# Performance work log

Hardware: AMD Instinct MI355X
Metric: run time of the kernel (lower is better)

The kernel has to match this reference:

```python
import jax, jax.numpy as jnp
import numpy as np

B, S, DIM = 4, 2048, 1024
E, K, H = 8, 2, 2048


def setup_inputs() -> dict:
    key = jax.random.key(0)
    ks = jax.random.split(key, 4)
    def init(k, shp, fan_in):
        return (jax.random.normal(k, shp, jnp.float32) / np.sqrt(fan_in)).astype(jnp.float32)
    return {
        "x": jax.random.normal(ks[0], (B, S, DIM), jnp.float32),
        "gate_w": init(ks[1], (DIM, E), DIM),
        "gate_b": jnp.zeros((E,), jnp.float32),
        "w1": init(ks[2], (E, DIM, H), DIM),
        "b1": jnp.zeros((E, H), jnp.float32),
        "w2": init(ks[3], (E, H, DIM), H),
        "b2": jnp.zeros((E, DIM), jnp.float32),
    }


def reference(x, gate_w, gate_b, w1, b1, w2, b2):
    orig_shape = x.shape
    xt = x.reshape(-1, orig_shape[-1])           # [N, D]
    N = xt.shape[0]

    logits = xt @ gate_w + gate_b                # [N, E]
    gate_weights = jax.nn.softmax(logits, axis=-1)
    top_w, top_i = jax.lax.top_k(gate_weights, K)           # [N, K]
    top_w = top_w / top_w.sum(axis=-1, keepdims=True)

    # combine weights: comb[n, e] = sum_k top_w[n,k] * (top_i[n,k] == e)
    comb = jnp.zeros((N, E), xt.dtype).at[jnp.arange(N)[:, None], top_i].add(top_w)

    # dense all-expert FFN (same math as masked gather/scatter loop)
    h = jax.nn.relu(jnp.einsum('nd,edh->neh', xt, w1) + b1)   # [N, E, H]
    out_e = jnp.einsum('neh,ehd->ned', h, w2) + b2            # [N, E, D]
    final = jnp.einsum('ne,ned->nd', comb, out_e).reshape(orig_shape)

    # load balancing loss
    usage = jnp.sum(jax.nn.one_hot(top_i, E, dtype=xt.dtype), axis=1)  # [N, E]
    expert_router_prob = gate_weights.sum(axis=0) / N
    expert_fraction_routed = usage.sum(axis=0) / N
    load_balancing_loss = jnp.sum(expert_router_prob * expert_fraction_routed)

    return final, load_balancing_loss
```

## Files before the change

kernel.cpp:

```cpp
#include <hip/hip_runtime.h>
#include <hip/hip_fp16.h>
#include <stdint.h>

#define N_TOK 8192
#define DIMD 1024
#define NEXP 8
#define HDIM 2048
#define BM 128
#define BN 128
#define BKK 64
#define MAXTILES 136
#define MAXROWS (MAXTILES * BM)
#define DUMPROW (2 * N_TOK)
#define CAP1 320
#define CAP2 160
#define G1 (8 * CAP1 + MAXTILES * 16)
#define G2 (8 * CAP2 + MAXTILES * 8)
#define TRB1 2048
#define TW2 2048
#define SMEM_BYTES 33024

typedef __attribute__((ext_vector_type(8))) short short8;
typedef __attribute__((ext_vector_type(4))) float f32x4;

__device__ __forceinline__ ushort f2bf(float f) {
    uint32_t u = __float_as_uint(f);
    u += 0x7fffu + ((u >> 16) & 1u);
    return (ushort)(u >> 16);
}

__device__ __forceinline__ void gload_lds16(const void* gsrc, void* lds_dst) {
    __builtin_amdgcn_global_load_lds(
        (const __attribute__((address_space(1))) void*)(uintptr_t)(gsrc),
        (__attribute__((address_space(3))) void*)(uintptr_t)(lds_dst),
        16, 0, 0);
}

__device__ __forceinline__ bool slot_map(const int* __restrict__ counts, int s,
                                         int NB, int CAP,
                                         int* e_out, int* tm_out, int* nb_out) {
    int ec[8], es[8], tot = 0;
#pragma unroll
    for (int e = 0; e < 8; e++) { es[e] = tot; ec[e] = (counts[e] + 127) >> 7; tot += ec[e]; }
    int aff = 8 * CAP;
    if (s < aff) {
        int e = s & 7, j = s >> 3;
        int need = ec[e] * NB;
        int lim = need < CAP ? need : CAP;
        if (j >= lim) return false;
        *e_out = e; *tm_out = es[e] + j / NB; *nb_out = j % NB;
        return true;
    }
    int O = s - aff, acc = 0;
#pragma unroll
    for (int e = 0; e < 8; e++) {
        int over = ec[e] * NB - CAP; if (over < 0) over = 0;
        if (O < acc + over) {
            int j = CAP + (O - acc);
            *e_out = e; *tm_out = es[e] + j / NB; *nb_out = j % NB;
            return true;
        }
        acc += over;
    }
    return false;
}

__device__ __forceinline__ void transpose_tile(const float* __restrict__ pin,
                                               ushort* __restrict__ pout,
                                               int R, int C, int rt, int ct,
                                               float (*t)[129], int tid) {
#pragma unroll
    for (int k = 0; k < 8; k++) {
        int q = tid + k * 256;
        int r = q >> 5, c4 = (q & 31) * 4;
        const float4 v = *(const float4*)(pin + (size_t)(rt * 64 + r) * C + ct * 128 + c4);
        t[r][c4] = v.x; t[r][c4 + 1] = v.y; t[r][c4 + 2] = v.z; t[r][c4 + 3] = v.w;
    }
    __syncthreads();
#pragma unroll
    for (int k = 0; k < 4; k++) {
        int p = tid + k * 256;
        int c = p >> 3, rs = (p & 7) * 8;
        alignas(16) ushort tmp[8];
#pragma unroll
        for (int j = 0; j < 8; j++) tmp[j] = f2bf(t[rs + j][c]);
        *(short8*)(pout + (size_t)(ct * 128 + c) * R + rt * 64 + rs) = *(const short8*)tmp;
    }
}


__global__ void prep_kernel(const float* __restrict__ w1, ushort* __restrict__ w1t,
                            const float* __restrict__ x, const float* __restrict__ gw,
                            const float* __restrict__ gb, int* __restrict__ topi,
                            float* __restrict__ topw, int* __restrict__ counts,
                            float* __restrict__ probsum, ushort* __restrict__ xb,
                            int* __restrict__ row_token, float* __restrict__ row_weight) {
    __shared__ alignas(16) char smem[SMEM_BYTES];
    int tid = threadIdx.x;
    if (blockIdx.x < TRB1) {
        int id = blockIdx.x;
        int e = id >> 8, tt = id & 255;
        int rt = tt >> 4, ct = tt & 15;
        transpose_tile(w1 + (size_t)e * DIMD * HDIM, w1t + (size_t)e * DIMD * HDIM,
                       DIMD, HDIM, rt, ct, (float(*)[129])smem, tid);
        return;
    }
    int gid = blockIdx.x - TRB1;
    float* ps = (float*)smem;
    int* cs = (int*)(smem + 64);
    if (gid < MAXROWS / 256) {
        int i = gid * 256 + tid;
        row_token[i] = DUMPROW; row_weight[i] = 0.f;
    }
    if (tid < NEXP) { ps[tid] = 0.f; cs[tid] = 0; }
    __syncthreads();
    int wid = tid >> 6, lane = tid & 63;
    int n = gid * 4 + wid;
    const float* xr = x + (size_t)n * DIMD;
    ushort* xbr = xb + (size_t)n * DIMD;
    float acc[NEXP];
#pragma unroll
    for (int e = 0; e < NEXP; e++) acc[e] = 0.f;
    for (int i = 0; i < DIMD / 64; i++) {
        int c = lane + i * 64;
        float xv = xr[c];
        xbr[c] = f2bf(xv);
        const float4* g4 = (const float4*)(gw + (size_t)c * NEXP);
        float4 ga = g4[0], gbv = g4[1];
        acc[0] += xv * ga.x;  acc[1] += xv * ga.y;
        acc[2] += xv * ga.z;  acc[3] += xv * ga.w;
        acc[4] += xv * gbv.x; acc[5] += xv * gbv.y;
        acc[6] += xv * gbv.z; acc[7] += xv * gbv.w;
    }
#pragma unroll
    for (int e = 0; e < NEXP; e++) {
        float v = acc[e];
#pragma unroll
        for (int off = 32; off > 0; off >>= 1) v += __shfl_xor(v, off);
        acc[e] = v + gb[e];
    }
    float m = acc[0];
#pragma unroll
    for (int e = 1; e < NEXP; e++) m = fmaxf(m, acc[e]);
    float p[NEXP], s = 0.f;
#pragma unroll
    for (int e = 0; e < NEXP; e++) { p[e] = expf(acc[e] - m); s += p[e]; }
    int e1 = 0;
#pragma unroll
    for (int e = 1; e < NEXP; e++) if (p[e] > p[e1]) e1 = e;
    int e2 = (e1 == 0) ? 1 : 0;
#pragma unroll
    for (int e = 0; e < NEXP; e++) if (e != e1 && p[e] > p[e2]) e2 = e;
    float wa = p[e1] / (p[e1] + p[e2]);
    if (lane == 0) {
        topi[n * 2] = e1; topi[n * 2 + 1] = e2;
        topw[n * 2] = wa; topw[n * 2 + 1] = 1.f - wa;
        atomicAdd(&cs[e1], 1); atomicAdd(&cs[e2], 1);
        float inv = 1.f / s;
#pragma unroll
        for (int e = 0; e < NEXP; e++) atomicAdd(&ps[e], p[e] * inv);
    }
    __syncthreads();
    if (tid < NEXP) { atomicAdd(&probsum[tid], ps[tid]); atomicAdd(&counts[tid], cs[tid]); }
}


__global__ void scatter_kernel(const int* __restrict__ topi, const float* __restrict__ topw,
                               const int* __restrict__ counts, int* __restrict__ cursor,
                               int* __restrict__ row_token, float* __restrict__ row_weight) {
    __shared__ int lcnt[NEXP], lbase[NEXP];
    int t = blockIdx.x * 256 + threadIdx.x;
    if (threadIdx.x < NEXP) lcnt[threadIdx.x] = 0;
    __syncthreads();
    int e = topi[t];
    int lpos = atomicAdd(&lcnt[e], 1);
    __syncthreads();
    if (threadIdx.x < NEXP) lbase[threadIdx.x] = atomicAdd(&cursor[threadIdx.x], lcnt[threadIdx.x]);
    __syncthreads();
    int pb = 0;
#pragma unroll
    for (int q = 0; q < NEXP; q++) {
        int rounded = ((counts[q] + 127) >> 7) << 7;
        pb += (q < e) ? rounded : 0;
    }
    int pos = pb + lbase[e] + lpos;
    row_token[pos] = t;
    row_weight[pos] = topw[t];
}


__global__ __launch_bounds__(256, 3) void gemm1_kernel(
        const ushort* __restrict__ xb, const ushort* __restrict__ w1t,
        const float* __restrict__ b1, ushort* __restrict__ hbuf,
        const int* __restrict__ row_token, const int* __restrict__ counts,
        const float* __restrict__ w2, ushort* __restrict__ w2t) {
    __shared__ alignas(16) char smem[SMEM_BYTES];
    ushort* ldsA = (ushort*)smem;
    ushort* ldsB = (ushort*)(smem + 16384);
    int tid = threadIdx.x;
    if (blockIdx.x >= G1) {
        int id = blockIdx.x - G1;
        int e = id >> 8, tt = id & 255;
        int rt = tt >> 3, ct = tt & 7;
        transpose_tile(w2 + (size_t)e * HDIM * DIMD, w2t + (size_t)e * HDIM * DIMD,
                       HDIM, DIMD, rt, ct, (float(*)[129])smem, tid);
        return;
    }
    int e, tm, nb;
    if (!slot_map(counts, blockIdx.x, 16, CAP1, &e, &tm, &nb)) return;
    int nbase = nb * BN;
    int slotbase = tm * BM;
    int lane = tid & 63, wid = tid >> 6;
    int wr = wid >> 1, wc = wid & 1;
    f32x4 acc[4][4];
#pragma unroll
    for (int i = 0; i < 4; i++)
#pragma unroll
        for (int j = 0; j < 4; j++) acc[i][j] = (f32x4){0.f, 0.f, 0.f, 0.f};
    int arow[4], acol[4], tok[4];
#pragma unroll
    for (int i = 0; i < 4; i++) {
        int p = i * 4096 + wid * 1024 + lane * 16;
        int row = p >> 7;
        int srclo = (p & 127) ^ ((row & 7) << 4);
        arow[i] = row; acol[i] = srclo >> 1;
        tok[i] = row_token[slotbase + row] >> 1;
    }
    const ushort* bmat = w1t + (size_t)e * HDIM * DIMD;
    const int NT = DIMD / BKK;

#pragma unroll
    for (int i = 0; i < 4; i++) {
        gload_lds16(xb + (size_t)tok[i] * DIMD + acol[i], ldsA + i * 2048 + wid * 512);
        gload_lds16(bmat + (size_t)(nbase + arow[i]) * DIMD + acol[i],
                    ldsB + i * 2048 + wid * 512);
    }
    __syncthreads();

    for (int kt = 0; kt < NT; kt++) {
        short8 af[4][2], bfv[4][2];
#pragma unroll
        for (int kk = 0; kk < 2; kk++) {
#pragma unroll
            for (int im = 0; im < 4; im++) {
                int row = wr * 64 + im * 16 + (lane & 15);
                int kbyte = kk * 64 + ((lane >> 4) * 16);
                af[im][kk] = *(const short8*)((const char*)ldsA +
                              row * 128 + (kbyte ^ ((row & 7) << 4)));
            }
#pragma unroll
            for (int in = 0; in < 4; in++) {
                int row = wc * 64 + in * 16 + (lane & 15);
                int kbyte = kk * 64 + ((lane >> 4) * 16);
                bfv[in][kk] = *(const short8*)((const char*)ldsB +
                               row * 128 + (kbyte ^ ((row & 7) << 4)));
            }
        }
        __syncthreads();
        if (kt + 1 < NT) {
            int k0 = (kt + 1) * BKK;
#pragma unroll
            for (int i = 0; i < 4; i++) {
                gload_lds16(xb + (size_t)tok[i] * DIMD + k0 + acol[i],
                            ldsA + i * 2048 + wid * 512);
                gload_lds16(bmat + (size_t)(nbase + arow[i]) * DIMD + k0 + acol[i],
                            ldsB + i * 2048 + wid * 512);
            }
        }
        __builtin_amdgcn_sched_barrier(0);
#pragma unroll
        for (int kk = 0; kk < 2; kk++)
#pragma unroll
            for (int im = 0; im < 4; im++)
#pragma unroll
                for (int in = 0; in < 4; in++)
                    acc[im][in] = __builtin_amdgcn_mfma_f32_16x16x32_bf16(
                        af[im][kk], bfv[in][kk], acc[im][in], 0, 0, 0);
        __syncthreads();
    }
    const float* b1e = b1 + (size_t)e * HDIM;
#pragma unroll
    for (int im = 0; im < 4; im++) {
#pragma unroll
        for (int in = 0; in < 4; in++) {
            int col = nbase + wc * 64 + in * 16 + (lane & 15);
            float bias = b1e[col];
#pragma unroll
            for (int r = 0; r < 4; r++) {
                int row = slotbase + wr * 64 + im * 16 + (lane >> 4) * 4 + r;
                float v = fmaxf(acc[im][in][r] + bias, 0.f);
                hbuf[(size_t)row * HDIM + col] = f2bf(v);
            }
        }
    }
}

__global__ __launch_bounds__(256, 3) void gemm2_kernel(
        const ushort* __restrict__ hbuf, const ushort* __restrict__ w2t,
        const float* __restrict__ b2, __half* __restrict__ pairbuf,
        const int* __restrict__ row_token, const float* __restrict__ row_weight,
        const int* __restrict__ counts) {
    int e, tm, nb;
    if (!slot_map(counts, blockIdx.x, 8, CAP2, &e, &tm, &nb)) return;
    int nbase = nb * BN;
    int slotbase = tm * BM;
    __shared__ alignas(16) ushort ldsA[BM * BKK];
    __shared__ alignas(16) ushort ldsB[BN * BKK];
    int tid = threadIdx.x, lane = tid & 63, wid = tid >> 6;
    int wr = wid >> 1, wc = wid & 1;
    f32x4 acc[4][4];
#pragma unroll
    for (int i = 0; i < 4; i++)
#pragma unroll
        for (int j = 0; j < 4; j++) acc[i][j] = (f32x4){0.f, 0.f, 0.f, 0.f};
    int arow[4], acol[4];
#pragma unroll
    for (int i = 0; i < 4; i++) {
        int p = i * 4096 + wid * 1024 + lane * 16;
        int row = p >> 7;
        int srclo = (p & 127) ^ ((row & 7) << 4);
        arow[i] = row; acol[i] = srclo >> 1;
    }
    const ushort* amat = hbuf + (size_t)slotbase * HDIM;
    const ushort* bmat = w2t + (size_t)e * DIMD * HDIM;
    const int NT = HDIM / BKK;

#pragma unroll
    for (int i = 0; i < 4; i++) {
        gload_lds16(amat + (size_t)arow[i] * HDIM + acol[i], &ldsA[i * 2048 + wid * 512]);
        gload_lds16(bmat + (size_t)(nbase + arow[i]) * HDIM + acol[i],
                    &ldsB[i * 2048 + wid * 512]);
    }
    __syncthreads();

    for (int kt = 0; kt < NT; kt++) {
        short8 af[4][2], bfv[4][2];
#pragma unroll
        for (int kk = 0; kk < 2; kk++) {
#pragma unroll
            for (int im = 0; im < 4; im++) {
                int row = wr * 64 + im * 16 + (lane & 15);
                int kbyte = kk * 64 + ((lane >> 4) * 16);
                af[im][kk] = *(const short8*)((const char*)ldsA +
                              row * 128 + (kbyte ^ ((row & 7) << 4)));
            }
#pragma unroll
            for (int in = 0; in < 4; in++) {
                int row = wc * 64 + in * 16 + (lane & 15);
                int kbyte = kk * 64 + ((lane >> 4) * 16);
                bfv[in][kk] = *(const short8*)((const char*)ldsB +
                               row * 128 + (kbyte ^ ((row & 7) << 4)));
            }
        }
        __syncthreads();
        if (kt + 1 < NT) {
            int k0 = (kt + 1) * BKK;
#pragma unroll
            for (int i = 0; i < 4; i++) {
                gload_lds16(amat + (size_t)arow[i] * HDIM + k0 + acol[i],
                            &ldsA[i * 2048 + wid * 512]);
                gload_lds16(bmat + (size_t)(nbase + arow[i]) * HDIM + k0 + acol[i],
                            &ldsB[i * 2048 + wid * 512]);
            }
        }
        __builtin_amdgcn_sched_barrier(0);
#pragma unroll
        for (int kk = 0; kk < 2; kk++)
#pragma unroll
            for (int im = 0; im < 4; im++)
#pragma unroll
                for (int in = 0; in < 4; in++)
                    acc[im][in] = __builtin_amdgcn_mfma_f32_16x16x32_bf16(
                        af[im][kk], bfv[in][kk], acc[im][in], 0, 0, 0);
        __syncthreads();
    }
    const float* b2e = b2 + (size_t)e * DIMD;
#pragma unroll
    for (int im = 0; im < 4; im++) {
#pragma unroll
        for (int r = 0; r < 4; r++) {
            int srow = slotbase + wr * 64 + im * 16 + (lane >> 4) * 4 + r;
            int pair = row_token[srow];
            float w = row_weight[srow];
            __half* prow = pairbuf + (size_t)pair * DIMD;
#pragma unroll
            for (int in = 0; in < 4; in++) {
                int col = nbase + wc * 64 + in * 16 + (lane & 15);
                float v = acc[im][in][r] + b2e[col];
                prow[col] = __float2half(w * v);
            }
        }
    }
}

__global__ void combine_kernel(const __half* __restrict__ pairbuf, float* __restrict__ outp,
                               const float* __restrict__ probsum, const int* __restrict__ counts) {
    int i = blockIdx.x * blockDim.x + threadIdx.x;
    int o = i * 8;
    int t = o >> 10, d = o & 1023;
    const __half* p0 = pairbuf + ((size_t)(t * 2) << 10) + d;
    const __half* p1 = p0 + DIMD;
    short8 h0 = *(const short8*)p0;
    short8 h1 = *(const short8*)p1;
    float4 r0, r1;
#pragma unroll
    for (int j = 0; j < 4; j++) {
        ((float*)&r0)[j] = __half2float(__ushort_as_half((ushort)h0[j])) +
                           __half2float(__ushort_as_half((ushort)h1[j]));
        ((float*)&r1)[j] = __half2float(__ushort_as_half((ushort)h0[j + 4])) +
                           __half2float(__ushort_as_half((ushort)h1[j + 4]));
    }
    float4* dst = (float4*)(outp + o);
    dst[0] = r0; dst[1] = r1;
    if (i == 0) {
        float l = 0.f;
#pragma unroll
        for (int e = 0; e < NEXP; e++) l += probsum[e] * (float)counts[e];
        outp[(size_t)N_TOK * DIMD] = l / ((float)N_TOK * (float)N_TOK);
    }
}


extern "C" void kernel_launch(void* const* d_in, const int* in_sizes, int n_in,
                              void* d_out, int out_size, void* d_ws, size_t ws_size,
                              hipStream_t stream) {
    const float* x      = (const float*)d_in[0];
    const float* gate_w = (const float*)d_in[1];
    const float* gate_b = (const float*)d_in[2];
    const float* w1     = (const float*)d_in[3];
    const float* b1     = (const float*)d_in[4];
    const float* w2     = (const float*)d_in[5];
    const float* b2     = (const float*)d_in[6];
    float* outp = (float*)d_out;

    char* ws = (char*)d_ws;
    ushort* xb   = (ushort*)(ws);
    ushort* w1t  = (ushort*)(ws + 16777216);
    ushort* w2t  = (ushort*)(ws + 50331648);
    ushort* hbuf = (ushort*)(ws + 83886080);
    __half* pairbuf = (__half*)(ws);
    char* ctrl   = ws + 155189248;
    int*   counts     = (int*)(ctrl + 0);
    int*   cursor     = (int*)(ctrl + 32);
    float* probsum    = (float*)(ctrl + 64);
    int*   topi       = (int*)(ctrl + 2048);
    float* topw       = (float*)(ctrl + 2048 + 65536);
    int*   row_token  = (int*)(ctrl + 2048 + 131072);
    float* row_weight = (float*)(ctrl + 2048 + 131072 + 69632);

    hipMemsetAsync(ctrl, 0, 128, stream);

    prep_kernel<<<TRB1 + N_TOK / 4, 256, 0, stream>>>(w1, w1t, x, gate_w, gate_b,
                                                      topi, topw, counts, probsum, xb,
                                                      row_token, row_weight);
    scatter_kernel<<<(N_TOK * 2) / 256, 256, 0, stream>>>(topi, topw, counts, cursor,
                                                          row_token, row_weight);
    gemm1_kernel<<<G1 + TW2, 256, 0, stream>>>(xb, w1t, b1, hbuf, row_token, counts,
                                               w2, w2t);
    gemm2_kernel<<<G2, 256, 0, stream>>>(hbuf, w2t, b2, pairbuf, row_token, row_weight, counts);
    combine_kernel<<<(N_TOK * DIMD / 8) / 256, 256, 0, stream>>>(pairbuf, outp,
                                                                 probsum, counts);
}
```

Baseline: 230.6 us.

## Enlarge GEMM M-tile to 256 rows with 512-thread blocks

Both expert GEMMs move from 128x128 tiles on 256 threads to 256x128 tiles on 512 threads (8 waves). Each wave still computes a 64x64 sub-tile, and the B tile is shared across more rows. The routing padding, the slot mapping, the workspace layout and the cooperative load indexing are all changed to the 256-row granularity. The intent is to reuse each loaded weight tile across twice as many rows and to cut per-block overhead. In exchange, padding waste per expert grows, there are fewer blocks, and LDS use per block rises, which may lower occupancy.

```diff
diff --git a/kernel.cpp b/kernel.cpp
--- a/kernel.cpp
+++ b/kernel.cpp
@@ -6,19 +6,19 @@
 #define DIMD 1024
 #define NEXP 8
 #define HDIM 2048
-#define BM 128
+#define BM 256
 #define BN 128
 #define BKK 64
-#define MAXTILES 136
-#define MAXROWS (MAXTILES * BM)
+#define MAXT 72
+#define MAXROWS (MAXT * 256)
 #define DUMPROW (2 * N_TOK)
-#define CAP1 320
-#define CAP2 160
-#define G1 (8 * CAP1 + MAXTILES * 16)
-#define G2 (8 * CAP2 + MAXTILES * 8)
+#define CAP1 160
+#define CAP2 80
+#define G1 (8 * CAP1 + MAXT * 16)
+#define G2 (8 * CAP2 + MAXT * 8)
 #define TRB1 2048
 #define TW2 2048
-#define SMEM_BYTES 33024
+#define SMEM1 49152
 
 typedef __attribute__((ext_vector_type(8))) short short8;
 typedef __attribute__((ext_vector_type(4))) float f32x4;
@@ -41,7 +41,7 @@
                                          int* e_out, int* tm_out, int* nb_out) {
     int ec[8], es[8], tot = 0;
 #pragma unroll
-    for (int e = 0; e < 8; e++) { es[e] = tot; ec[e] = (counts[e] + 127) >> 7; tot += ec[e]; }
+    for (int e = 0; e < 8; e++) { es[e] = tot; ec[e] = (counts[e] + 255) >> 8; tot += ec[e]; }
     int aff = 8 * CAP;
     if (s < aff) {
         int e = s & 7, j = s >> 3;
@@ -68,18 +68,14 @@
 __device__ __forceinline__ void transpose_tile(const float* __restrict__ pin,
                                                ushort* __restrict__ pout,
                                                int R, int C, int rt, int ct,
-                                               float (*t)[129], int tid) {
-#pragma unroll
-    for (int k = 0; k < 8; k++) {
-        int q = tid + k * 256;
+                                               float (*t)[129], int tid, int NTH) {
+    for (int q = tid; q < 2048; q += NTH) {
         int r = q >> 5, c4 = (q & 31) * 4;
         const float4 v = *(const float4*)(pin + (size_t)(rt * 64 + r) * C + ct * 128 + c4);
         t[r][c4] = v.x; t[r][c4 + 1] = v.y; t[r][c4 + 2] = v.z; t[r][c4 + 3] = v.w;
     }
     __syncthreads();
-#pragma unroll
-    for (int k = 0; k < 4; k++) {
-        int p = tid + k * 256;
+    for (int p = tid; p < 1024; p += NTH) {
         int c = p >> 3, rs = (p & 7) * 8;
         alignas(16) ushort tmp[8];
 #pragma unroll
@@ -95,14 +91,14 @@
                             float* __restrict__ topw, int* __restrict__ counts,
                             float* __restrict__ probsum, ushort* __restrict__ xb,
                             int* __restrict__ row_token, float* __restrict__ row_weight) {
-    __shared__ alignas(16) char smem[SMEM_BYTES];
+    __shared__ alignas(16) char smem[33024];
     int tid = threadIdx.x;
     if (blockIdx.x < TRB1) {
         int id = blockIdx.x;
         int e = id >> 8, tt = id & 255;
         int rt = tt >> 4, ct = tt & 15;
         transpose_tile(w1 + (size_t)e * DIMD * HDIM, w1t + (size_t)e * DIMD * HDIM,
-                       DIMD, HDIM, rt, ct, (float(*)[129])smem, tid);
+                       DIMD, HDIM, rt, ct, (float(*)[129])smem, tid, 256);
         return;
     }
     int gid = blockIdx.x - TRB1;
@@ -180,7 +176,7 @@
     int pb = 0;
 #pragma unroll
     for (int q = 0; q < NEXP; q++) {
-        int rounded = ((counts[q] + 127) >> 7) << 7;
+        int rounded = ((counts[q] + 255) >> 8) << 8;
         pb += (q < e) ? rounded : 0;
     }
     int pos = pb + lbase[e] + lpos;
@@ -189,21 +185,21 @@
 }
 
 
-__global__ __launch_bounds__(256, 3) void gemm1_kernel(
+__global__ __launch_bounds__(512, 4) void gemm1_kernel(
         const ushort* __restrict__ xb, const ushort* __restrict__ w1t,
         const float* __restrict__ b1, ushort* __restrict__ hbuf,
         const int* __restrict__ row_token, const int* __restrict__ counts,
         const float* __restrict__ w2, ushort* __restrict__ w2t) {
-    __shared__ alignas(16) char smem[SMEM_BYTES];
+    __shared__ alignas(16) char smem[SMEM1];
     ushort* ldsA = (ushort*)smem;
-    ushort* ldsB = (ushort*)(smem + 16384);
+    ushort* ldsB = (ushort*)(smem + 32768);
     int tid = threadIdx.x;
     if (blockIdx.x >= G1) {
         int id = blockIdx.x - G1;
         int e = id >> 8, tt = id & 255;
         int rt = tt >> 3, ct = tt & 7;
         transpose_tile(w2 + (size_t)e * HDIM * DIMD, w2t + (size_t)e * HDIM * DIMD,
-                       HDIM, DIMD, rt, ct, (float(*)[129])smem, tid);
+                       HDIM, DIMD, rt, ct, (float(*)[129])smem, tid, 512);
         return;
     }
     int e, tm, nb;
@@ -217,24 +213,22 @@
     for (int i = 0; i < 4; i++)
 #pragma unroll
         for (int j = 0; j < 4; j++) acc[i][j] = (f32x4){0.f, 0.f, 0.f, 0.f};
-    int arow[4], acol[4], tok[4];
-#pragma unroll
-    for (int i = 0; i < 4; i++) {
-        int p = i * 4096 + wid * 1024 + lane * 16;
-        int row = p >> 7;
-        int srclo = (p & 127) ^ ((row & 7) << 4);
-        arow[i] = row; acol[i] = srclo >> 1;
-        tok[i] = row_token[slotbase + row] >> 1;
-    }
+    int srow = tid >> 3;
+    int scol = ((((tid & 7) * 16) ^ ((srow & 7) << 4)) >> 1);
+    int tok[4];
+#pragma unroll
+    for (int i = 0; i < 4; i++)
+        tok[i] = row_token[slotbase + i * 64 + srow] >> 1;
     const ushort* bmat = w1t + (size_t)e * HDIM * DIMD;
     const int NT = DIMD / BKK;
 
 #pragma unroll
-    for (int i = 0; i < 4; i++) {
-        gload_lds16(xb + (size_t)tok[i] * DIMD + acol[i], ldsA + i * 2048 + wid * 512);
-        gload_lds16(bmat + (size_t)(nbase + arow[i]) * DIMD + acol[i],
-                    ldsB + i * 2048 + wid * 512);
-    }
+    for (int i = 0; i < 4; i++)
+        gload_lds16(xb + (size_t)tok[i] * DIMD + scol, ldsA + i * 4096 + tid * 8);
+#pragma unroll
+    for (int i = 0; i < 2; i++)
+        gload_lds16(bmat + (size_t)(nbase + i * 64 + srow) * DIMD + scol,
+                    ldsB + i * 4096 + tid * 8);
     __syncthreads();
 
     for (int kt = 0; kt < NT; kt++) {
@@ -260,12 +254,13 @@
         if (kt + 1 < NT) {
             int k0 = (kt + 1) * BKK;
 #pragma unroll
-            for (int i = 0; i < 4; i++) {
-                gload_lds16(xb + (size_t)tok[i] * DIMD + k0 + acol[i],
-                            ldsA + i * 2048 + wid * 512);
-                gload_lds16(bmat + (size_t)(nbase + arow[i]) * DIMD + k0 + acol[i],
-                            ldsB + i * 2048 + wid * 512);
-            }
+            for (int i = 0; i < 4; i++)
+                gload_lds16(xb + (size_t)tok[i] * DIMD + k0 + scol,
+                            ldsA + i * 4096 + tid * 8);
+#pragma unroll
+            for (int i = 0; i < 2; i++)
+                gload_lds16(bmat + (size_t)(nbase + i * 64 + srow) * DIMD + k0 + scol,
+                            ldsB + i * 4096 + tid * 8);
         }
         __builtin_amdgcn_sched_barrier(0);
 #pragma unroll
@@ -295,7 +290,7 @@
     }
 }
 
-__global__ __launch_bounds__(256, 3) void gemm2_kernel(
+__global__ __launch_bounds__(512, 4) void gemm2_kernel(
         const ushort* __restrict__ hbuf, const ushort* __restrict__ w2t,
         const float* __restrict__ b2, __half* __restrict__ pairbuf,
         const int* __restrict__ row_token, const float* __restrict__ row_weight,
@@ -313,24 +308,19 @@
     for (int i = 0; i < 4; i++)
 #pragma unroll
         for (int j = 0; j < 4; j++) acc[i][j] = (f32x4){0.f, 0.f, 0.f, 0.f};
-    int arow[4], acol[4];
-#pragma unroll
-    for (int i = 0; i < 4; i++) {
-        int p = i * 4096 + wid * 1024 + lane * 16;
-        int row = p >> 7;
-        int srclo = (p & 127) ^ ((row & 7) << 4);
-        arow[i] = row; acol[i] = srclo >> 1;
-    }
+    int srow = tid >> 3;
+    int scol = ((((tid & 7) * 16) ^ ((srow & 7) << 4)) >> 1);
     const ushort* amat = hbuf + (size_t)slotbase * HDIM;
     const ushort* bmat = w2t + (size_t)e * DIMD * HDIM;
     const int NT = HDIM / BKK;
 
 #pragma unroll
-    for (int i = 0; i < 4; i++) {
-        gload_lds16(amat + (size_t)arow[i] * HDIM + acol[i], &ldsA[i * 2048 + wid * 512]);
-        gload_lds16(bmat + (size_t)(nbase + arow[i]) * HDIM + acol[i],
-                    &ldsB[i * 2048 + wid * 512]);
-    }
+    for (int i = 0; i < 4; i++)
+        gload_lds16(amat + (size_t)(i * 64 + srow) * HDIM + scol, ldsA + i * 4096 + tid * 8);
+#pragma unroll
+    for (int i = 0; i < 2; i++)
+        gload_lds16(bmat + (size_t)(nbase + i * 64 + srow) * HDIM + scol,
+                    ldsB + i * 4096 + tid * 8);
     __syncthreads();
 
     for (int kt = 0; kt < NT; kt++) {
@@ -356,12 +346,13 @@
         if (kt + 1 < NT) {
             int k0 = (kt + 1) * BKK;
 #pragma unroll
-            for (int i = 0; i < 4; i++) {
-                gload_lds16(amat + (size_t)arow[i] * HDIM + k0 + acol[i],
-                            &ldsA[i * 2048 + wid * 512]);
-                gload_lds16(bmat + (size_t)(nbase + arow[i]) * HDIM + k0 + acol[i],
-                            &ldsB[i * 2048 + wid * 512]);
-            }
+            for (int i = 0; i < 4; i++)
+                gload_lds16(amat + (size_t)(i * 64 + srow) * HDIM + k0 + scol,
+                            ldsA + i * 4096 + tid * 8);
+#pragma unroll
+            for (int i = 0; i < 2; i++)
+                gload_lds16(bmat + (size_t)(nbase + i * 64 + srow) * HDIM + k0 + scol,
+                            ldsB + i * 4096 + tid * 8);
         }
         __builtin_amdgcn_sched_barrier(0);
 #pragma unroll
@@ -379,9 +370,9 @@
     for (int im = 0; im < 4; im++) {
 #pragma unroll
         for (int r = 0; r < 4; r++) {
-            int srow = slotbase + wr * 64 + im * 16 + (lane >> 4) * 4 + r;
-            int pair = row_token[srow];
-            float w = row_weight[srow];
+            int srw = slotbase + wr * 64 + im * 16 + (lane >> 4) * 4 + r;
+            int pair = row_token[srw];
+            float w = row_weight[srw];
             __half* prow = pairbuf + (size_t)pair * DIMD;
 #pragma unroll
             for (int in = 0; in < 4; in++) {
@@ -439,14 +430,14 @@
     ushort* w2t  = (ushort*)(ws + 50331648);
     ushort* hbuf = (ushort*)(ws + 83886080);
     __half* pairbuf = (__half*)(ws);
-    char* ctrl   = ws + 155189248;
+    char* ctrl   = ws + 159383552;
     int*   counts     = (int*)(ctrl + 0);
     int*   cursor     = (int*)(ctrl + 32);
     float* probsum    = (float*)(ctrl + 64);
     int*   topi       = (int*)(ctrl + 2048);
     float* topw       = (float*)(ctrl + 2048 + 65536);
     int*   row_token  = (int*)(ctrl + 2048 + 131072);
-    float* row_weight = (float*)(ctrl + 2048 + 131072 + 69632);
+    float* row_weight = (float*)(ctrl + 2048 + 131072 + 73728);
 
     hipMemsetAsync(ctrl, 0, 128, stream);
 
@@ -455,9 +446,9 @@
                                                       row_token, row_weight);
     scatter_kernel<<<(N_TOK * 2) / 256, 256, 0, stream>>>(topi, topw, counts, cursor,
                                                           row_token, row_weight);
-    gemm1_kernel<<<G1 + TW2, 256, 0, stream>>>(xb, w1t, b1, hbuf, row_token, counts,
+    gemm1_kernel<<<G1 + TW2, 512, 0, stream>>>(xb, w1t, b1, hbuf, row_token, counts,
                                                w2, w2t);
-    gemm2_kernel<<<G2, 256, 0, stream>>>(hbuf, w2t, b2, pairbuf, row_token, row_weight, counts);
+    gemm2_kernel<<<G2, 512, 0, stream>>>(hbuf, w2t, b2, pairbuf, row_token, row_weight, counts);
     combine_kernel<<<(N_TOK * DIMD / 8) / 256, 256, 0, stream>>>(pairbuf, outp,
                                                                  probsum, counts);
 }
```

Measured after the change: 588.3 us. 155% more time.
